# Performance work log

Hardware: AMD Instinct MI355X
Metric: run time of the kernel (lower is better)

Reference implementation:

```python
import jax, jax.numpy as jnp
import numpy as np

D, H, L, P = 256, 8, 3, 4
DH = D // H
SHAPES = np.array([[72, 96], [36, 48], [18, 24]], dtype=np.int64)
STARTS = np.array([0, 72 * 96, 72 * 96 + 36 * 48], dtype=np.int64)
NV = int((SHAPES[:, 0] * SHAPES[:, 1]).sum())  # 9072


def layer_norm(x, s, b):
    m = x.mean(-1, keepdims=True)
    v = ((x - m) ** 2).mean(-1, keepdims=True)
    return (x - m) / jnp.sqrt(v + 1e-5) * s + b


def bilinear(v, loc, Hl, Wl):
    # v: [B,H,Hl*Wl,dh]; loc: [B,Lq,H,P,2] normalized in [0,1]
    B, nH, _, dh = v.shape
    Lq, nP = loc.shape[1], loc.shape[3]
    x = loc[..., 0] * Wl - 0.5  # grid_sample align_corners=False
    y = loc[..., 1] * Hl - 0.5
    x0 = jnp.floor(x); y0 = jnp.floor(y)
    wx = x - x0; wy = y - y0

    def gather(xi, yi, w):
        valid = (xi >= 0) & (xi < Wl) & (yi >= 0) & (yi < Hl)  # padding_mode='zeros'
        xi_c = jnp.clip(xi, 0, Wl - 1).astype(jnp.int32)
        yi_c = jnp.clip(yi, 0, Hl - 1).astype(jnp.int32)
        idx = jnp.transpose(yi_c * Wl + xi_c, (0, 2, 1, 3)).reshape(B, nH, Lq * nP)
        g = jnp.take_along_axis(v, idx[..., None], axis=2).reshape(B, nH, Lq, nP, dh)
        m = (jnp.transpose(valid, (0, 2, 1, 3)).astype(v.dtype) * jnp.transpose(w, (0, 2, 1, 3)))[..., None]
        return g * m

    return (gather(x0, y0, (1 - wx) * (1 - wy)) + gather(x0 + 1, y0, wx * (1 - wy))
            + gather(x0, y0 + 1, (1 - wx) * wy) + gather(x0 + 1, y0 + 1, wx * wy))


def ms_deform_attn(query, value_in, spatial_shapes, level_start_index, key_padding_mask,
                   ref, off_w, off_b, aw_w, aw_b, vproj_w, vproj_b, oproj_w, oproj_b):
    B, Lq, _ = query.shape
    off = (query @ off_w + off_b).reshape(B, Lq, H, L, P, 2)
    aw = jax.nn.softmax((query @ aw_w + aw_b).reshape(B, Lq, H, L * P), axis=-1).reshape(B, Lq, H, L, P)
    # normalizer is [W_l, H_l] per level
    normalizer = jnp.asarray(np.stack([SHAPES[:, 1], SHAPES[:, 0]], axis=-1), dtype=query.dtype)  # [L,2]
    loc = ref[:, :, None, :, None, :] + off / normalizer[None, None, None, :, None, :]  # [B,Lq,H,L,P,2]
    value = value_in @ vproj_w + vproj_b
    value = jnp.where(key_padding_mask[:, :, None], 0.0, value)
    value = value.reshape(B, -1, H, DH).transpose(0, 2, 1, 3)  # [B,H,Nv,dh]
    acc = 0.0
    for l in range(L):
        Hl, Wl = int(spatial_shapes[l][0]), int(spatial_shapes[l][1])
        st = int(level_start_index[l])
        v_l = value[:, :, st:st + Hl * Wl]
        sampled = bilinear(v_l, loc[:, :, :, l], Hl, Wl)  # [B,H,Lq,P,dh]
        acc = acc + (sampled * jnp.transpose(aw[:, :, :, l], (0, 2, 1, 3))[..., None]).sum(axis=3)
    ctx = acc.transpose(0, 2, 1, 3).reshape(B, Lq, D)
    return ctx @ oproj_w + oproj_b


def mha(q_in, kv_in, key_padding_mask, qw, qb, kw, kb, vw, vb, ow, ob):
    B, Lq, _ = q_in.shape
    Lk = kv_in.shape[1]
    q = (q_in @ qw + qb).reshape(B, Lq, H, DH)
    k = (kv_in @ kw + kb).reshape(B, Lk, H, DH)
    v = (kv_in @ vw + vb).reshape(B, Lk, H, DH)
    scores = jnp.einsum('bqhd,bkhd->bhqk', q, k) / jnp.sqrt(jnp.asarray(DH, q.dtype))
    scores = jnp.where(key_padding_mask[:, None, None, :], -1e9, scores)
    a = jax.nn.softmax(scores, axis=-1)
    ctx = jnp.einsum('bhqk,bkhd->bqhd', a, v).reshape(B, Lq, D)
    return ctx @ ow + ob


def _forward(vis_tokens, text_tokens, vis_value,
             ref_w, ref_b, off_w, off_b, aw_w, aw_b, vproj_w, vproj_b, oproj_w, oproj_b,
             lvi_out_w, lvi_out_b, lvi_n1_s, lvi_n1_b, lvi_f1_w, lvi_f1_b, lvi_f2_w, lvi_f2_b, lvi_n2_s, lvi_n2_b,
             mha_qw, mha_qb, mha_kw, mha_kb, mha_vw, mha_vb, mha_ow, mha_ob,
             vli_out_w, vli_out_b, vli_n1_s, vli_n1_b, vli_f1_w, vli_f1_b, vli_f2_w, vli_f2_b, vli_n2_s, vli_n2_b,
             spatial_shapes, level_start_index, text_padding_mask, vis_key_padding_mask):
    B, Lt, _ = text_tokens.shape
    # --- DeformLVI: text queries multi-scale visual features ---
    ref = jax.nn.sigmoid(text_tokens @ ref_w + ref_b).reshape(B, Lt, L, 2)
    ctx = ms_deform_attn(text_tokens, vis_value, spatial_shapes, level_start_index, vis_key_padding_mask,
                         ref, off_w, off_b, aw_w, aw_b, vproj_w, vproj_b, oproj_w, oproj_b)
    t = layer_norm(text_tokens + ctx @ lvi_out_w + lvi_out_b, lvi_n1_s, lvi_n1_b)
    ffn = jax.nn.relu(t @ lvi_f1_w + lvi_f1_b) @ lvi_f2_w + lvi_f2_b
    text_out = layer_norm(t + ffn, lvi_n2_s, lvi_n2_b)
    # --- VLI: visual tokens query enriched text ---
    ctx_v = mha(vis_tokens, text_out, text_padding_mask, mha_qw, mha_qb, mha_kw, mha_kb, mha_vw, mha_vb, mha_ow, mha_ob)
    v = layer_norm(vis_tokens + ctx_v @ vli_out_w + vli_out_b, vli_n1_s, vli_n1_b)
    ffn_v = jax.nn.relu(v @ vli_f1_w + vli_f1_b) @ vli_f2_w + vli_f2_b
    vis_out = layer_norm(v + ffn_v, vli_n2_s, vli_n2_b)
    return vis_out, text_out


def setup_inputs() -> dict:
    key = jax.random.key(0)
    ks = iter(jax.random.split(key, 64))
    B, Lt = 8, 32
    w = lambda i, o: jax.random.normal(next(ks), (i, o), jnp.float32) * 0.02
    z = lambda o: jnp.zeros((o,), jnp.float32)
    inp = {
        'vis_tokens': jax.random.normal(next(ks), (B, NV, D), jnp.float32),
        'text_tokens': jax.random.normal(next(ks), (B, Lt, D), jnp.float32),
        'vis_value': jax.random.normal(next(ks), (B, NV, D), jnp.float32),
        'ref_w': w(D, L * 2), 'ref_b': z(L * 2),
        'off_w': w(D, H * L * P * 2), 'off_b': z(H * L * P * 2),
        'aw_w': w(D, H * L * P), 'aw_b': z(H * L * P),
        'vproj_w': w(D, D), 'vproj_b': z(D),
        'oproj_w': w(D, D), 'oproj_b': z(D),
        'lvi_out_w': w(D, D), 'lvi_out_b': z(D),
        'lvi_n1_s': jnp.ones((D,), jnp.float32), 'lvi_n1_b': z(D),
        'lvi_f1_w': w(D, 4 * D), 'lvi_f1_b': z(4 * D),
        'lvi_f2_w': w(4 * D, D), 'lvi_f2_b': z(D),
        'lvi_n2_s': jnp.ones((D,), jnp.float32), 'lvi_n2_b': z(D),
        'mha_qw': w(D, D), 'mha_qb': z(D),
        'mha_kw': w(D, D), 'mha_kb': z(D),
        'mha_vw': w(D, D), 'mha_vb': z(D),
        'mha_ow': w(D, D), 'mha_ob': z(D),
        'vli_out_w': w(D, D), 'vli_out_b': z(D),
        'vli_n1_s': jnp.ones((D,), jnp.float32), 'vli_n1_b': z(D),
        'vli_f1_w': w(D, 4 * D), 'vli_f1_b': z(4 * D),
        'vli_f2_w': w(4 * D, D), 'vli_f2_b': z(D),
        'vli_n2_s': jnp.ones((D,), jnp.float32), 'vli_n2_b': z(D),
        'spatial_shapes': SHAPES,
        'level_start_index': STARTS,
        'text_padding_mask': jnp.zeros((B, Lt), bool),
        'vis_key_padding_mask': jnp.zeros((B, NV), bool),
    }
    return inp


def reference(vis_tokens, text_tokens, vis_value,
              ref_w, ref_b, off_w, off_b, aw_w, aw_b, vproj_w, vproj_b, oproj_w, oproj_b,
              lvi_out_w, lvi_out_b, lvi_n1_s, lvi_n1_b, lvi_f1_w, lvi_f1_b, lvi_f2_w, lvi_f2_b, lvi_n2_s, lvi_n2_b,
              mha_qw, mha_qb, mha_kw, mha_kb, mha_vw, mha_vb, mha_ow, mha_ob,
              vli_out_w, vli_out_b, vli_n1_s, vli_n1_b, vli_f1_w, vli_f1_b, vli_f2_w, vli_f2_b, vli_n2_s, vli_n2_b,
              spatial_shapes, level_start_index, text_padding_mask, vis_key_padding_mask):
    return _forward(vis_tokens, text_tokens, vis_value,
                    ref_w, ref_b, off_w, off_b, aw_w, aw_b, vproj_w, vproj_b, oproj_w, oproj_b,
                    lvi_out_w, lvi_out_b, lvi_n1_s, lvi_n1_b, lvi_f1_w, lvi_f1_b, lvi_f2_w, lvi_f2_b, lvi_n2_s, lvi_n2_b,
                    mha_qw, mha_qb, mha_kw, mha_kb, mha_vw, mha_vb, mha_ow, mha_ob,
                    vli_out_w, vli_out_b, vli_n1_s, vli_n1_b, vli_f1_w, vli_f1_b, vli_f2_w, vli_f2_b, vli_n2_s, vli_n2_b,
                    spatial_shapes, level_start_index, text_padding_mask, vis_key_padding_mask)
```

## Files before the change

### kernel.cpp

```cpp
#include <hip/hip_runtime.h>
#include <hip/hip_bf16.h>
#include <math.h>

typedef __hip_bfloat16 bf16;
typedef unsigned short ushort_t;
typedef unsigned int uint_t;
typedef short v8s __attribute__((ext_vector_type(8)));
typedef float v4f __attribute__((ext_vector_type(4)));

#define NVTOK 9072
#define BATCH 8
#define LT 32
#define DMODEL 256
#define NHEAD 8
#define DHEAD 32
#define MVIS (BATCH*NVTOK)
#define MTEXT (BATCH*LT)
#define VISSZ 18579456ull

__device__ __forceinline__ float bf2f(ushort_t u){ return __uint_as_float(((uint_t)u)<<16); }
__device__ __forceinline__ ushort_t f2bfbits(float f){
  __hip_bfloat16 h = __float2bfloat16(f);
  union { __hip_bfloat16 h; ushort_t u; } c; c.h = h; return c.u;
}
__device__ __forceinline__ float ldin(const void* p, size_t i, int mode){
  return mode ? ((const float*)p)[i] : bf2f(((const ushort_t*)p)[i]);
}
__device__ __forceinline__ void stout(void* p, size_t i, int mode, float v){
  if (mode) ((float*)p)[i] = v; else ((ushort_t*)p)[i] = f2bfbits(v);
}

__device__ __forceinline__ void gload_lds16(const void* g, void* l){
  __builtin_amdgcn_global_load_lds(
      (const __attribute__((address_space(1))) unsigned int*)g,
      (__attribute__((address_space(3))) unsigned int*)l, 16, 0, 0);
}

__global__ void k_detect(const uint_t* __restrict__ buf, int n_avail, int* __restrict__ flag){
  __shared__ int zc, bc;
  if (threadIdx.x==0){ zc=0; bc=0; }
  __syncthreads();
  int stride = n_avail/2048; if (stride < 1) stride = 1;
  int nz=0, nb=0;
  for (int i=threadIdx.x; i<2048; i+=256){
    long long idx = (long long)i*stride;
    if (idx >= n_avail) break;
    uint_t d = buf[idx];
    uint_t lo = d & 0xFFFFu;
    int e = (int)((lo >> 7) & 0xFF);
    if (lo == 0) nz++;
    else if (e >= 90 && e <= 160) nb++;
  }
  atomicAdd(&zc, nz); atomicAdd(&bc, nb);
  __syncthreads();
  if (threadIdx.x==0){
    int mode;
    if (zc > 1024) mode = 1;
    else if (bc > 1228) mode = 0;
    else mode = 1;
    *flag = mode;
  }
}

__global__ __launch_bounds__(256) void k_transpose(
    const void* W, ushort_t* __restrict__ Wt, int K, int N,
    const int* __restrict__ mf)
{
  const int mode = *mf;
  __shared__ float tile[32][33];
  const int k0 = blockIdx.x*32, n0 = blockIdx.y*32;
  const int c = threadIdx.x & 31, r8 = threadIdx.x >> 5;
  #pragma unroll
  for (int i=0;i<4;i++){
    const int kk = r8 + i*8;
    tile[kk][c] = ldin(W, (size_t)(k0+kk)*N + n0 + c, mode);
  }
  __syncthreads();
  #pragma unroll
  for (int i=0;i<4;i++){
    const int nn = r8 + i*8;
    Wt[(size_t)(n0+nn)*K + k0 + c] = f2bfbits(tile[c][nn]);
  }
}

__global__ __launch_bounds__(256) void k_text_prep(
    const void* text,
    const void* ref_w, const void* ref_b,
    const void* off_w, const void* off_b,
    const void* aw_w,  const void* aw_b,
    float* __restrict__ loc_out, float* __restrict__ aw_out,
    const int* __restrict__ mf)
{
  const int mode = *mf;
  const int r = blockIdx.x;
  const int t = threadIdx.x;
  __shared__ float x[256];
  __shared__ float refv[6];
  __shared__ float offv[192];
  __shared__ float logit[96];
  x[t] = ldin(text, (size_t)r*256 + t, mode);
  __syncthreads();
  if (t < 192) {
    float s = 0.f;
    for (int k=0;k<256;k++) s += x[k]*ldin(off_w, (size_t)k*192+t, mode);
    offv[t] = s + ldin(off_b, t, mode);
  } else if (t < 198) {
    int j = t-192;
    float s = 0.f;
    for (int k=0;k<256;k++) s += x[k]*ldin(ref_w, (size_t)k*6+j, mode);
    s += ldin(ref_b, j, mode);
    refv[j] = 1.f/(1.f+expf(-s));
  }
  if (t < 96) {
    float s = 0.f;
    for (int k=0;k<256;k++) s += x[k]*ldin(aw_w, (size_t)k*96+t, mode);
    logit[t] = s + ldin(aw_b, t, mode);
  }
  __syncthreads();
  if (t < 8) {
    float mx = -1e30f;
    for (int j=0;j<12;j++) mx = fmaxf(mx, logit[t*12+j]);
    float e[12]; float den = 0.f;
    for (int j=0;j<12;j++){ e[j] = expf(logit[t*12+j]-mx); den += e[j]; }
    float inv = 1.f/den;
    for (int j=0;j<12;j++) aw_out[(size_t)r*96 + t*12 + j] = e[j]*inv;
  }
  if (t < 192) {
    int rem = t % 24;
    int l = rem >> 3;
    int c = t & 1;
    const float normW[3] = {96.f,48.f,24.f};
    const float normH[3] = {72.f,36.f,18.f};
    float nrm = (c==0) ? normW[l] : normH[l];
    loc_out[(size_t)r*192 + t] = refv[l*2+c] + offv[t]/nrm;
  }
}

__global__ __launch_bounds__(64) void k_deform(
    const void* vis_value, const char* __restrict__ vmask,
    const void* vproj_w, const void* vproj_b,
    const float* __restrict__ loc, const float* __restrict__ aw,
    float* __restrict__ ctx_out, const int* __restrict__ mf)
{
  const int mode = *mf;
  const int blk = blockIdx.x;
  const int r = blk >> 3;
  const int h = blk & 7;
  const int b = r >> 5;
  const int t = threadIdx.x;
  const int Hs[3] = {72,36,18};
  const int Wsz[3] = {96,48,24};
  const int stl[3] = {0,6912,8640};
  float s0=0.f,s1=0.f,s2=0.f,s3=0.f, wsum=0.f;
  for (int l=0;l<3;l++){
    for (int p=0;p<4;p++){
      const int sIdx = blk*12 + l*4 + p;
      const float a  = aw[sIdx];
      const float X = loc[sIdx*2+0]*(float)Wsz[l] - 0.5f;
      const float Y = loc[sIdx*2+1]*(float)Hs[l] - 0.5f;
      const float x0f = floorf(X), y0f = floorf(Y);
      const int x0 = (int)x0f, y0 = (int)y0f;
      const float wx = X-x0f, wy = Y-y0f;
      const float cw[4] = {(1.f-wx)*(1.f-wy), wx*(1.f-wy), (1.f-wx)*wy, wx*wy};
      const int cx[4] = {x0,x0+1,x0,x0+1};
      const int cy[4] = {y0,y0,y0+1,y0+1};
      for (int c=0;c<4;c++){
        if (cx[c]>=0 && cx[c]<Wsz[l] && cy[c]>=0 && cy[c]<Hs[l]){
          const size_t pos = (size_t)b*NVTOK + stl[l] + cy[c]*Wsz[l] + cx[c];
          if (vmask[pos]) continue;
          const float w = a*cw[c];
          wsum += w;
          const size_t base = pos*256 + t*4;
          s0 += w*ldin(vis_value, base+0, mode);
          s1 += w*ldin(vis_value, base+1, mode);
          s2 += w*ldin(vis_value, base+2, mode);
          s3 += w*ldin(vis_value, base+3, mode);
        }
      }
    }
  }
  __shared__ float sh[256];
  sh[t*4+0]=s0; sh[t*4+1]=s1; sh[t*4+2]=s2; sh[t*4+3]=s3;
  __syncthreads();
  if (t < 32) {
    const int col = h*32 + t;
    float acc = wsum * ldin(vproj_b, col, mode);
    for (int k=0;k<256;k++) acc += sh[k]*ldin(vproj_w, (size_t)k*256+col, mode);
    ctx_out[(size_t)r*256 + col] = acc;
  }
}

__device__ __forceinline__ float block_sum(float v, float* red){
  float sm = v;
  #pragma unroll
  for (int o=32;o>0;o>>=1) sm += __shfl_down(sm,o);
  const int t = threadIdx.x;
  __syncthreads();
  if ((t&63)==0) red[t>>6] = sm;
  __syncthreads();
  return red[0]+red[1]+red[2]+red[3];
}

__global__ __launch_bounds__(256) void k_mgemm(
    const void* A, size_t a_off, int a_kind,
    const ushort_t* __restrict__ Wt, const void* bias, float* __restrict__ C,
    int N, int K, int relu, const int* __restrict__ mf)
{
  const int mode = *mf;
  const int split = (a_kind==1) || (mode==1);
  __shared__ ushort_t Ah[128*32];
  __shared__ ushort_t Al[128*32];
  __shared__ ushort_t Bt[128*32];
  const int tid = threadIdx.x;
  const int gm0 = blockIdx.x*128, gn0 = blockIdx.y*128;
  const int wv = tid>>6, lane = tid&63;
  const int mh = (wv&1)*64, nh = (wv>>1)*64;
  const int r16 = lane&15, q8 = (lane>>4)*8;
  const int srow = tid>>1, sseg = (tid&1)*16;
  v4f acc[4][4];
  #pragma unroll
  for (int i=0;i<4;i++)
    #pragma unroll
    for (int j=0;j<4;j++) acc[i][j] = (v4f){0.f,0.f,0.f,0.f};

  for (int k0=0; k0<K; k0+=32){
    if (k0) __syncthreads();
    {
      const ushort_t* src = Wt + (size_t)(gn0+srow)*K + k0 + sseg;
      ((uint4*)&Bt[srow*32+sseg])[0]   = ((const uint4*)src)[0];
      ((uint4*)&Bt[srow*32+sseg+8])[0] = ((const uint4*)src)[1];
    }
    if (!split){
      const ushort_t* src = (const ushort_t*)A + a_off + (size_t)(gm0+srow)*K + k0 + sseg;
      ((uint4*)&Ah[srow*32+sseg])[0]   = ((const uint4*)src)[0];
      ((uint4*)&Ah[srow*32+sseg+8])[0] = ((const uint4*)src)[1];
    } else {
      const float* src = (const float*)A + a_off + (size_t)(gm0+srow)*K + k0 + sseg;
      #pragma unroll
      for (int v=0;v<4;v++){
        float4 f = ((const float4*)src)[v];
        float xs[4] = {f.x, f.y, f.z, f.w};
        #pragma unroll
        for (int e=0;e<4;e++){
          const int idx = srow*32 + sseg + v*4 + e;
          const ushort_t h = f2bfbits(xs[e]);
          Ah[idx] = h;
          Al[idx] = f2bfbits(xs[e] - bf2f(h));
        }
      }
    }
    __syncthreads();
    v8s af[4], bfr[4], al[4];
    #pragma unroll
    for (int mt=0;mt<4;mt++){
      af[mt] = *(const v8s*)&Ah[(mh + mt*16 + r16)*32 + q8];
      if (split) al[mt] = *(const v8s*)&Al[(mh + mt*16 + r16)*32 + q8];
    }
    #pragma unroll
    for (int nt=0;nt<4;nt++)
      bfr[nt] = *(const v8s*)&Bt[(nh + nt*16 + r16)*32 + q8];
    #pragma unroll
    for (int mt=0;mt<4;mt++){
      #pragma unroll
      for (int nt=0;nt<4;nt++){
        acc[mt][nt] = __builtin_amdgcn_mfma_f32_16x16x32_bf16(af[mt], bfr[nt], acc[mt][nt], 0, 0, 0);
        if (split)
          acc[mt][nt] = __builtin_amdgcn_mfma_f32_16x16x32_bf16(al[mt], bfr[nt], acc[mt][nt], 0, 0, 0);
      }
    }
  }
  const int rq = (lane>>4)*4;
  float bv[4];
  #pragma unroll
  for (int nt=0;nt<4;nt++) bv[nt] = ldin(bias, gn0 + nh + nt*16 + r16, mode);
  #pragma unroll
  for (int mt=0;mt<4;mt++){
    #pragma unroll
    for (int r=0;r<4;r++){
      const size_t ro = (size_t)(gm0 + mh + mt*16 + rq + r)*N + gn0 + nh + r16;
      #pragma unroll
      for (int nt=0;nt<4;nt++){
        float v = acc[mt][nt][r] + bv[nt];
        if (relu) v = fmaxf(v, 0.f);
        C[ro + nt*16] = v;
      }
    }
  }
}

__global__ __launch_bounds__(256) void k_mgemm3(
    const void* A, size_t a_off, int a_kind,
    const ushort_t* __restrict__ Wt, const void* bias,
    float* __restrict__ Cf, ushort_t* __restrict__ Chi,
    int N, int K, int relu, const int* __restrict__ mf)
{
  const int mode = *mf;
  const int rawf32 = (a_kind==0) && (mode==1);
  __shared__ ushort_t Ah[128*32];
  __shared__ ushort_t Bt[128*32];
  const int tid = threadIdx.x;
  const int nbx = gridDim.x, nby = gridDim.y;
  const int total = nbx*nby;
  const int f = blockIdx.y*nbx + blockIdx.x;
  const int qq = total>>3, rr = total&7;
  const int xcd = f&7, pos = f>>3;
  const int wg = (xcd<rr ? xcd*(qq+1) : rr*(qq+1) + (xcd-rr)*qq) + pos;
  const int gm0 = (wg / nby)*128, gn0 = (wg % nby)*128;

  const int wv = tid>>6, lane = tid&63;
  const int mh = (wv&1)*64, nh = (wv>>1)*64;
  const int r16 = lane&15, q8 = (lane>>4)*8;
  const int grow = tid>>2;
  const int gcol = (tid&3)*8;
  const int srow = tid>>1, sseg = (tid&1)*16;
  const ushort_t* Abf = (const ushort_t*)A + a_off;
  v4f acc[4][4];
  #pragma unroll
  for (int i=0;i<4;i++)
    #pragma unroll
    for (int j=0;j<4;j++) acc[i][j] = (v4f){0.f,0.f,0.f,0.f};

  for (int k0=0; k0<K; k0+=32){
    if (k0) __syncthreads();
    gload_lds16(Wt + (size_t)(gn0+grow)*K    + k0 + gcol, &Bt[grow*32      + gcol]);
    gload_lds16(Wt + (size_t)(gn0+grow+64)*K + k0 + gcol, &Bt[(grow+64)*32 + gcol]);
    if (!rawf32){
      gload_lds16(Abf + (size_t)(gm0+grow)*K    + k0 + gcol, &Ah[grow*32      + gcol]);
      gload_lds16(Abf + (size_t)(gm0+grow+64)*K + k0 + gcol, &Ah[(grow+64)*32 + gcol]);
    } else {
      const float* src = (const float*)A + a_off + (size_t)(gm0+srow)*K + k0 + sseg;
      #pragma unroll
      for (int v=0;v<4;v++){
        float4 fq = ((const float4*)src)[v];
        float xs[4] = {fq.x, fq.y, fq.z, fq.w};
        #pragma unroll
        for (int e=0;e<4;e++)
          Ah[srow*32 + sseg + v*4 + e] = f2bfbits(xs[e]);
      }
    }
    __syncthreads();
    v8s af[4], bfr[4];
    #pragma unroll
    for (int mt=0;mt<4;mt++)
      af[mt] = *(const v8s*)&Ah[(mh + mt*16 + r16)*32 + q8];
    #pragma unroll
    for (int nt=0;nt<4;nt++)
      bfr[nt] = *(const v8s*)&Bt[(nh + nt*16 + r16)*32 + q8];
    #pragma unroll
    for (int mt=0;mt<4;mt++){
      #pragma unroll
      for (int nt=0;nt<4;nt++)
        acc[mt][nt] = __builtin_amdgcn_mfma_f32_16x16x32_bf16(af[mt], bfr[nt], acc[mt][nt], 0, 0, 0);
    }
  }
  const int rq = (lane>>4)*4;
  float bv[4];
  #pragma unroll
  for (int nt=0;nt<4;nt++) bv[nt] = ldin(bias, gn0 + nh + nt*16 + r16, mode);
  const int outf = (Cf != nullptr);
  #pragma unroll
  for (int mt=0;mt<4;mt++){
    #pragma unroll
    for (int r=0;r<4;r++){
      const size_t ro = (size_t)(gm0 + mh + mt*16 + rq + r)*N + gn0 + nh + r16;
      #pragma unroll
      for (int nt=0;nt<4;nt++){
        float v = acc[mt][nt][r] + bv[nt];
        if (relu) v = fmaxf(v, 0.f);
        if (outf) Cf[ro + nt*16] = v;
        else      Chi[ro + nt*16] = f2bfbits(v);
      }
    }
  }
}

__global__ __launch_bounds__(256) void k_kvsplit(
    const float* __restrict__ kws, const float* __restrict__ vws,
    ushort_t* __restrict__ khi, ushort_t* __restrict__ klo,
    ushort_t* __restrict__ vthi, ushort_t* __restrict__ vtlo)
{
  const int row = blockIdx.x;
  const int b = row >> 5, key = row & 31;
  const int t = threadIdx.x;
  const float f = kws[(size_t)row*256 + t];
  const ushort_t fh = f2bfbits(f);
  khi[(size_t)row*256 + t] = fh;
  klo[(size_t)row*256 + t] = f2bfbits(f - bf2f(fh));
  const float g = vws[(size_t)row*256 + t];
  const ushort_t gh = f2bfbits(g);
  const size_t vt = ((size_t)b*256 + t)*32 + key;
  vthi[vt] = gh;
  vtlo[vt] = f2bfbits(g - bf2f(gh));
}

__global__ __launch_bounds__(256) void k_attn2(
    const ushort_t* __restrict__ qcH,
    ushort_t* __restrict__ aoh,
    const ushort_t* __restrict__ khi, const ushort_t* __restrict__ klo,
    const ushort_t* __restrict__ vthi, const ushort_t* __restrict__ vtlo,
    const char* __restrict__ tmask, int r0)
{
  __shared__ float P[4][16][36];
  const int tid = threadIdx.x;
  const int wv = tid>>6, lane = tid&63;
  const int lrow0 = blockIdx.x*64 + wv*16;
  const int b = (r0 + lrow0)/NVTOK;
  const int m16 = lane&15;
  const int kq = lane>>4;
  const int q8 = kq*8;
  const int key0 = m16, key1 = m16+16;
  const bool msk0 = tmask[b*LT + key0] != 0;
  const bool msk1 = tmask[b*LT + key1] != 0;
  const float scale = 0.17677669529663687f;

  for (int h=0; h<8; ++h){
    const size_t qoff = (size_t)(lrow0 + m16)*256 + h*32 + q8;
    const v8s qh = *(const v8s*)&qcH[qoff];
    const size_t kb0 = ((size_t)(b*32+key0)*256) + h*32 + q8;
    const size_t kb1 = ((size_t)(b*32+key1)*256) + h*32 + q8;
    const v8s kh0 = *(const v8s*)&khi[kb0];
    const v8s kl0 = *(const v8s*)&klo[kb0];
    const v8s kh1 = *(const v8s*)&khi[kb1];
    const v8s kl1 = *(const v8s*)&klo[kb1];
    v4f s0 = (v4f){0.f,0.f,0.f,0.f}, s1 = (v4f){0.f,0.f,0.f,0.f};
    s0 = __builtin_amdgcn_mfma_f32_16x16x32_bf16(qh, kh0, s0, 0,0,0);
    s0 = __builtin_amdgcn_mfma_f32_16x16x32_bf16(qh, kl0, s0, 0,0,0);
    s1 = __builtin_amdgcn_mfma_f32_16x16x32_bf16(qh, kh1, s1, 0,0,0);
    s1 = __builtin_amdgcn_mfma_f32_16x16x32_bf16(qh, kl1, s1, 0,0,0);
    float e0[4], e1[4], inv[4];
    #pragma unroll
    for (int r=0;r<4;r++){
      const float a0 = msk0 ? -1e9f : s0[r]*scale;
      const float a1 = msk1 ? -1e9f : s1[r]*scale;
      float mx = fmaxf(a0,a1);
      #pragma unroll
      for (int o=1;o<16;o<<=1) mx = fmaxf(mx, __shfl_xor(mx,o));
      const float x0 = __expf(a0-mx), x1 = __expf(a1-mx);
      float dn = x0+x1;
      #pragma unroll
      for (int o=1;o<16;o<<=1) dn += __shfl_xor(dn,o);
      e0[r]=x0; e1[r]=x1; inv[r] = 1.f/dn;
    }
    #pragma unroll
    for (int r=0;r<4;r++){
      P[wv][kq*4+r][key0] = e0[r];
      P[wv][kq*4+r][key1] = e1[r];
    }
    __syncthreads();
    float pv[8];
    *(float4*)&pv[0] = *(const float4*)&P[wv][m16][q8];
    *(float4*)&pv[4] = *(const float4*)&P[wv][m16][q8+4];
    v8s ph;
    #pragma unroll
    for (int j=0;j<8;j++) ph[j] = (short)f2bfbits(pv[j]);
    const size_t vb0 = ((size_t)(b*256 + h*32 + m16)*32) + q8;
    const size_t vb1 = ((size_t)(b*256 + h*32 + 16 + m16)*32) + q8;
    const v8s vh0 = *(const v8s*)&vthi[vb0];
    const v8s vl0 = *(const v8s*)&vtlo[vb0];
    const v8s vh1 = *(const v8s*)&vthi[vb1];
    const v8s vl1 = *(const v8s*)&vtlo[vb1];
    v4f o0 = (v4f){0.f,0.f,0.f,0.f}, o1 = (v4f){0.f,0.f,0.f,0.f};
    o0 = __builtin_amdgcn_mfma_f32_16x16x32_bf16(ph, vh0, o0, 0,0,0);
    o0 = __builtin_amdgcn_mfma_f32_16x16x32_bf16(ph, vl0, o0, 0,0,0);
    o1 = __builtin_amdgcn_mfma_f32_16x16x32_bf16(ph, vh1, o1, 0,0,0);
    o1 = __builtin_amdgcn_mfma_f32_16x16x32_bf16(ph, vl1, o1, 0,0,0);
    __syncthreads();
    #pragma unroll
    for (int r=0;r<4;r++){
      const size_t ro = (size_t)(lrow0 + kq*4 + r)*256 + h*32;
      aoh[ro + m16]      = f2bfbits(o0[r]*inv[r]);
      aoh[ro + 16 + m16] = f2bfbits(o1[r]*inv[r]);
    }
  }
}

__global__ __launch_bounds__(256) void k_add_ln(
    const float* __restrict__ X, const void* R, size_t r_off, int r_f32,
    void* OUT, size_t o_off, int o_f32,
    void* OUT2, size_t o2_off,
    const void* g, const void* be, const int* __restrict__ mf)
{
  const int mode = *mf;
  const int row = blockIdx.x; const int t = threadIdx.x;
  const size_t idx = (size_t)row*256 + t;
  __shared__ float red[4];
  const float rv = r_f32 ? ((const float*)R)[r_off+idx] : ldin(R, r_off+idx, mode);
  const float v = X[idx] + rv;
  const float m = block_sum(v, red) * (1.f/256.f);
  __syncthreads();
  const float d = v - m;
  const float var = block_sum(d*d, red) * (1.f/256.f);
  const float o = d*rsqrtf(var+1e-5f)*ldin(g,t,mode) + ldin(be,t,mode);
  if (o_f32) ((float*)OUT)[o_off+idx] = o;
  else       stout(OUT, o_off+idx, mode, o);
  if (OUT2)  stout(OUT2, o2_off+idx, mode, o);
}

__global__ __launch_bounds__(256) void k_add_ln_h(
    const float* __restrict__ X, const void* R, size_t r_off,
    ushort_t* __restrict__ OH,
    const void* g, const void* be, const int* __restrict__ mf)
{
  const int mode = *mf;
  const int row = blockIdx.x; const int t = threadIdx.x;
  const size_t idx = (size_t)row*256 + t;
  __shared__ float red[4];
  const float rv = ldin(R, r_off+idx, mode);
  const float v = X[idx] + rv;
  const float m = block_sum(v, red) * (1.f/256.f);
  __syncthreads();
  const float d = v - m;
  const float var = block_sum(d*d, red) * (1.f/256.f);
  const float o = d*rsqrtf(var+1e-5f)*ldin(g,t,mode) + ldin(be,t,mode);
  OH[idx] = f2bfbits(o);
}

__global__ __launch_bounds__(256) void k_add_ln_pres(
    const float* __restrict__ X,
    const ushort_t* __restrict__ RH,
    void* OUT, size_t o_off,
    const void* g, const void* be, const int* __restrict__ mf)
{
  const int mode = *mf;
  const int row = blockIdx.x; const int t = threadIdx.x;
  const size_t idx = (size_t)row*256 + t;
  __shared__ float red[4];
  const float rv = bf2f(RH[idx]);
  const float v = X[idx] + rv;
  const float m = block_sum(v, red) * (1.f/256.f);
  __syncthreads();
  const float d = v - m;
  const float var = block_sum(d*d, red) * (1.f/256.f);
  const float o = d*rsqrtf(var+1e-5f)*ldin(g,t,mode) + ldin(be,t,mode);
  stout(OUT, o_off+idx, mode, o);
}

extern "C" void kernel_launch(void* const* d_in, const int* in_sizes, int n_in,
                              void* d_out, int out_size, void* d_ws, size_t ws_size,
                              hipStream_t stream)
{
  (void)n_in; (void)out_size;
  const void* vis_tokens = d_in[0];
  const void* text_tokens= d_in[1];
  const void* vis_value  = d_in[2];
  const void* ref_w = d_in[3];  const void* ref_b = d_in[4];
  const void* off_w = d_in[5];  const void* off_b = d_in[6];
  const void* aw_w  = d_in[7];  const void* aw_b  = d_in[8];
  const void* vproj_w = d_in[9];  const void* vproj_b = d_in[10];
  const void* oproj_w = d_in[11]; const void* oproj_b = d_in[12];
  const void* lvi_out_w = d_in[13]; const void* lvi_out_b = d_in[14];
  const void* lvi_n1_s = d_in[15];  const void* lvi_n1_b = d_in[16];
  const void* lvi_f1_w = d_in[17];  const void* lvi_f1_b = d_in[18];
  const void* lvi_f2_w = d_in[19];  const void* lvi_f2_b = d_in[20];
  const void* lvi_n2_s = d_in[21];  const void* lvi_n2_b = d_in[22];
  const void* mha_qw = d_in[23]; const void* mha_qb = d_in[24];
  const void* mha_kw = d_in[25]; const void* mha_kb = d_in[26];
  const void* mha_vw = d_in[27]; const void* mha_vb = d_in[28];
  const void* mha_ow = d_in[29]; const void* mha_ob = d_in[30];
  const void* vli_out_w = d_in[31]; const void* vli_out_b = d_in[32];
  const void* vli_n1_s = d_in[33];  const void* vli_n1_b = d_in[34];
  const void* vli_f1_w = d_in[35];  const void* vli_f1_b = d_in[36];
  const void* vli_f2_w = d_in[37];  const void* vli_f2_b = d_in[38];
  const void* vli_n2_s = d_in[39];  const void* vli_n2_b = d_in[40];
  const char* tmask = (const char*)d_in[43];
  const char* vmask = (const char*)d_in[44];

  char* ws = (char*)d_ws;
  int*   flag    = (int*)  (ws + 0);
  float* loc_ws  = (float*)(ws + 256);
  float* aw_ws   = (float*)(ws + 196864);
  float* ctxt_ws = (float*)(ws + 295168);
  float* t_ws    = (float*)(ws + 557312);
  float* tout_ws = (float*)(ws + 819456);
  float* k_ws    = (float*)(ws + 1081600);
  float* v_ws    = (float*)(ws + 1343744);
  ushort_t* wtq  = (ushort_t*)(ws + 1605888ull);
  ushort_t* wto  = (ushort_t*)(ws + 1736960ull);
  ushort_t* wtf1 = (ushort_t*)(ws + 1868032ull);
  ushort_t* wtf2 = (ushort_t*)(ws + 2392320ull);
  ushort_t* wtk   = (ushort_t*)(ws + 2916608ull);
  ushort_t* wtv   = (ushort_t*)(ws + 3047680ull);
  ushort_t* wtop  = (ushort_t*)(ws + 3178752ull);
  ushort_t* wtlo  = (ushort_t*)(ws + 3309824ull);
  ushort_t* wtlf1 = (ushort_t*)(ws + 3440896ull);
  ushort_t* wtlf2 = (ushort_t*)(ws + 3965184ull);
  float* hbuf_t   = (float*)(ws + 4489472ull);
  float* ybuf     = (float*)(ws + 5538048ull);
  float* fbuf     = (float*)(ws + 5800192ull);
  ushort_t* khi   = (ushort_t*)(ws + 6062336ull);
  ushort_t* klo   = (ushort_t*)(ws + 6193408ull);
  ushort_t* vthi  = (ushort_t*)(ws + 6324480ull);
  ushort_t* vtlo  = (ushort_t*)(ws + 6455552ull);
  const size_t fe = 6586624ull;

  long long R_ll = 128;
  if (ws_size > fe) R_ll = (long long)((ws_size - fe) / 3584ull);
  if (R_ll > (long long)MVIS) R_ll = MVIS;
  R_ll &= ~127LL;
  if (R_ll < 128) R_ll = 128;
  const int R = (int)R_ll;
  ushort_t* qcH  = (ushort_t*)(ws + fe);
  float*    ubuf = (float*)   (ws + fe);
  ushort_t* v1H  = (ushort_t*)(ws + fe + (size_t)R*1024ull);
  ushort_t* hbH  = (ushort_t*)(ws + fe + (size_t)R*1536ull);
  ushort_t* aoH  = hbH;

  int ndw = in_sizes[1]/2; if (ndw < 1) ndw = 1;
  k_detect<<<1,256,0,stream>>>((const uint_t*)text_tokens, ndw, flag);

  k_transpose<<<dim3(8,8),  256,0,stream>>>(mha_qw,    wtq,   256, 256,  flag);
  k_transpose<<<dim3(8,8),  256,0,stream>>>(mha_ow,    wto,   256, 256,  flag);
  k_transpose<<<dim3(8,32), 256,0,stream>>>(vli_f1_w,  wtf1,  256, 1024, flag);
  k_transpose<<<dim3(32,8), 256,0,stream>>>(vli_f2_w,  wtf2,  1024, 256, flag);
  k_transpose<<<dim3(8,8),  256,0,stream>>>(mha_kw,    wtk,   256, 256,  flag);
  k_transpose<<<dim3(8,8),  256,0,stream>>>(mha_vw,    wtv,   256, 256,  flag);
  k_transpose<<<dim3(8,8),  256,0,stream>>>(oproj_w,   wtop,  256, 256,  flag);
  k_transpose<<<dim3(8,8),  256,0,stream>>>(lvi_out_w, wtlo,  256, 256,  flag);
  k_transpose<<<dim3(8,32), 256,0,stream>>>(lvi_f1_w,  wtlf1, 256, 1024, flag);
  k_transpose<<<dim3(32,8), 256,0,stream>>>(lvi_f2_w,  wtlf2, 1024, 256, flag);

  k_text_prep<<<MTEXT,256,0,stream>>>(text_tokens, ref_w, ref_b, off_w, off_b,
                                      aw_w, aw_b, loc_ws, aw_ws, flag);
  k_deform<<<MTEXT*NHEAD,64,0,stream>>>(vis_value, vmask, vproj_w, vproj_b,
                                        loc_ws, aw_ws, ctxt_ws, flag);

  {
    dim3 g22(2,2);
    k_mgemm<<<g22,256,0,stream>>>(ctxt_ws, 0, 1, wtop, oproj_b, ybuf, 256, 256, 0, flag);
    k_mgemm<<<g22,256,0,stream>>>(ybuf,    0, 1, wtlo, lvi_out_b, fbuf, 256, 256, 0, flag);
    k_add_ln<<<MTEXT,256,0,stream>>>(fbuf, text_tokens, 0, 0,
                                     t_ws, 0, 1, nullptr, 0, lvi_n1_s, lvi_n1_b, flag);
  }
  {
    dim3 g28(2,8), g22(2,2);
    k_mgemm<<<g28,256,0,stream>>>(t_ws,   0, 1, wtlf1, lvi_f1_b, hbuf_t, 1024, 256, 1, flag);
    k_mgemm<<<g22,256,0,stream>>>(hbuf_t, 0, 1, wtlf2, lvi_f2_b, fbuf,   256, 1024, 0, flag);
    k_add_ln<<<MTEXT,256,0,stream>>>(fbuf, t_ws, 0, 1,
                                     tout_ws, 0, 1, d_out, VISSZ, lvi_n2_s, lvi_n2_b, flag);
  }
  {
    dim3 g22(2,2);
    k_mgemm<<<g22,256,0,stream>>>(tout_ws, 0, 1, wtk, mha_kb, k_ws, 256, 256, 0, flag);
    k_mgemm<<<g22,256,0,stream>>>(tout_ws, 0, 1, wtv, mha_vb, v_ws, 256, 256, 0, flag);
    k_kvsplit<<<256,256,0,stream>>>(k_ws, v_ws, khi, klo, vthi, vtlo);
  }

  for (int r0 = 0; r0 < MVIS; r0 += R){
    const int nr = (MVIS - r0 < R) ? (MVIS - r0) : R;
    dim3 g2(nr/128, 2);
    k_mgemm3<<<g2,256,0,stream>>>(vis_tokens, (size_t)r0*256, 0,
                                  wtq, mha_qb, nullptr, qcH, 256, 256, 0, flag);
    k_attn2<<<nr/64,256,0,stream>>>(qcH, aoH, khi, klo, vthi, vtlo, tmask, r0);
    k_mgemm3<<<g2,256,0,stream>>>(aoH, 0, 2,
                                  wto, mha_ob, ubuf, nullptr, 256, 256, 0, flag);
    k_add_ln_h<<<nr,256,0,stream>>>(ubuf, vis_tokens, (size_t)r0*256,
                                    v1H, vli_n1_s, vli_n1_b, flag);
    dim3 g8(nr/128, 8);
    k_mgemm3<<<g8,256,0,stream>>>(v1H, 0, 2,
                                  wtf1, vli_f1_b, nullptr, hbH, 1024, 256, 1, flag);
    k_mgemm3<<<g2,256,0,stream>>>(hbH, 0, 2,
                                  wtf2, vli_f2_b, ubuf, nullptr, 256, 1024, 0, flag);
    k_add_ln_pres<<<nr,256,0,stream>>>(ubuf, v1H,
                                       d_out, (size_t)r0*256, vli_n2_s, vli_n2_b, flag);
  }
}
```

Measured before the change: 883.6 us.

## Fuse vision FFN up and down projections into one kernel keeping hidden in LDS

Replaces the two FFN GEMM launches (256->1024 with ReLU, then 1024->256) with a single kernel that computes each 128-column slice of the hidden activation, stores it as bf16 in swizzled shared memory, and immediately accumulates it into the output projection. This removes the round trip of the 1024-wide hidden buffer through global memory and shrinks per-row workspace so larger row chunks fit. In exchange each 128-row block does all the work with only nr/128 blocks of 512 threads, which lowers parallelism and re-reads the input and weight fragments from global memory for each hidden slice.

```diff
diff --git a/kernel.cpp b/kernel.cpp
--- a/kernel.cpp
+++ b/kernel.cpp
@@ -374,6 +374,99 @@
   }
 }
 
+__global__ __launch_bounds__(512) void k_ffn(
+    const ushort_t* __restrict__ X,
+    const ushort_t* __restrict__ W1t,
+    const void* b1,
+    const ushort_t* __restrict__ W2t,
+    const void* b2,
+    float* __restrict__ Y,
+    const int* __restrict__ mf)
+{
+  const int mode = *mf;
+  __shared__ ushort_t h[128*128];
+  const int tid = threadIdx.x;
+  const int wv = tid>>6, lane = tid&63;
+  const int r16 = lane&15, kq = lane>>4, q8 = kq*8;
+  const int rh = (wv&1)*64;
+  const int cs = (wv>>1)*32;
+  const int cq = (wv>>1)*64;
+  const int gm0 = blockIdx.x*128;
+  v4f yacc[4][4];
+  #pragma unroll
+  for (int i=0;i<4;i++)
+    #pragma unroll
+    for (int j=0;j<4;j++) yacc[i][j] = (v4f){0.f,0.f,0.f,0.f};
+
+  for (int j=0; j<8; ++j){
+    v4f hacc[4][2];
+    #pragma unroll
+    for (int i=0;i<4;i++){ hacc[i][0]=(v4f){0.f,0.f,0.f,0.f}; hacc[i][1]=(v4f){0.f,0.f,0.f,0.f}; }
+    #pragma unroll
+    for (int k=0;k<8;++k){
+      v8s af[4], bf[2];
+      #pragma unroll
+      for (int mt=0;mt<4;mt++)
+        af[mt] = *(const v8s*)&X[(size_t)(gm0 + rh + mt*16 + r16)*256 + k*32 + q8];
+      #pragma unroll
+      for (int nt=0;nt<2;nt++)
+        bf[nt] = *(const v8s*)&W1t[(size_t)(j*128 + cs + nt*16 + r16)*256 + k*32 + q8];
+      #pragma unroll
+      for (int mt=0;mt<4;mt++)
+        #pragma unroll
+        for (int nt=0;nt<2;nt++)
+          hacc[mt][nt] = __builtin_amdgcn_mfma_f32_16x16x32_bf16(af[mt], bf[nt], hacc[mt][nt], 0,0,0);
+    }
+    if (j) __syncthreads();
+    #pragma unroll
+    for (int nt=0;nt<2;nt++){
+      const int col = cs + nt*16 + r16;
+      const float bb = ldin(b1, j*128 + col, mode);
+      const int c2hi = (col*2) & ~15, c2lo = (col*2) & 15;
+      #pragma unroll
+      for (int mt=0;mt<4;mt++){
+        #pragma unroll
+        for (int r=0;r<4;r++){
+          const int row = rh + mt*16 + kq*4 + r;
+          const float v = fmaxf(hacc[mt][nt][r] + bb, 0.f);
+          const int byte = row*256 + (c2hi ^ ((row&7)<<4)) + c2lo;
+          h[byte>>1] = f2bfbits(v);
+        }
+      }
+    }
+    __syncthreads();
+    #pragma unroll
+    for (int kk=0;kk<4;++kk){
+      v8s af2[4], bf2[4];
+      #pragma unroll
+      for (int mt=0;mt<4;mt++){
+        const int row = rh + mt*16 + r16;
+        const int byte = row*256 + (((kk*32 + q8)*2) ^ ((row&7)<<4));
+        af2[mt] = *(const v8s*)&h[byte>>1];
+      }
+      #pragma unroll
+      for (int nt=0;nt<4;nt++)
+        bf2[nt] = *(const v8s*)&W2t[(size_t)(cq + nt*16 + r16)*1024 + j*128 + kk*32 + q8];
+      #pragma unroll
+      for (int mt=0;mt<4;mt++)
+        #pragma unroll
+        for (int nt=0;nt<4;nt++)
+          yacc[mt][nt] = __builtin_amdgcn_mfma_f32_16x16x32_bf16(af2[mt], bf2[nt], yacc[mt][nt], 0,0,0);
+    }
+  }
+  const int rq = kq*4;
+  #pragma unroll
+  for (int nt=0;nt<4;nt++){
+    const float bb = ldin(b2, cq + nt*16 + r16, mode);
+    #pragma unroll
+    for (int mt=0;mt<4;mt++){
+      #pragma unroll
+      for (int r=0;r<4;r++)
+        Y[(size_t)(gm0 + rh + mt*16 + rq + r)*256 + cq + nt*16 + r16] = yacc[mt][nt][r] + bb;
+    }
+  }
+}
+
 __global__ __launch_bounds__(256) void k_kvsplit(
     const float* __restrict__ kws, const float* __restrict__ vws,
     ushort_t* __restrict__ khi, ushort_t* __restrict__ klo,
@@ -594,7 +687,7 @@
   const size_t fe = 6586624ull;
 
   long long R_ll = 128;
-  if (ws_size > fe) R_ll = (long long)((ws_size - fe) / 3584ull);
+  if (ws_size > fe) R_ll = (long long)((ws_size - fe) / 2048ull);
   if (R_ll > (long long)MVIS) R_ll = MVIS;
   R_ll &= ~127LL;
   if (R_ll < 128) R_ll = 128;
@@ -602,8 +695,7 @@
   ushort_t* qcH  = (ushort_t*)(ws + fe);
   float*    ubuf = (float*)   (ws + fe);
   ushort_t* v1H  = (ushort_t*)(ws + fe + (size_t)R*1024ull);
-  ushort_t* hbH  = (ushort_t*)(ws + fe + (size_t)R*1536ull);
-  ushort_t* aoH  = hbH;
+  ushort_t* aoH  = (ushort_t*)(ws + fe + (size_t)R*1536ull);
 
   int ndw = in_sizes[1]/2; if (ndw < 1) ndw = 1;
   k_detect<<<1,256,0,stream>>>((const uint_t*)text_tokens, ndw, flag);
@@ -655,11 +747,7 @@
                                   wto, mha_ob, ubuf, nullptr, 256, 256, 0, flag);
     k_add_ln_h<<<nr,256,0,stream>>>(ubuf, vis_tokens, (size_t)r0*256,
                                     v1H, vli_n1_s, vli_n1_b, flag);
-    dim3 g8(nr/128, 8);
-    k_mgemm3<<<g8,256,0,stream>>>(v1H, 0, 2,
-                                  wtf1, vli_f1_b, nullptr, hbH, 1024, 256, 1, flag);
-    k_mgemm3<<<g2,256,0,stream>>>(hbH, 0, 2,
-                                  wtf2, vli_f2_b, ubuf, nullptr, 256, 1024, 0, flag);
+    k_ffn<<<nr/128,512,0,stream>>>(v1H, wtf1, vli_f1_b, wtf2, vli_f2_b, ubuf, flag);
     k_add_ln_pres<<<nr,256,0,stream>>>(ubuf, v1H,
                                        d_out, (size_t)r0*256, vli_n2_s, vli_n2_b, flag);
   }
```

Result: slower. 1.136 ms (+28.5%).

## Fuse residual add and LayerNorm into full-row GEMM epilogue

Applied to the files above, without the earlier changes.

Adds a GEMM kernel with 512 threads that computes a full 128x256 output tile, adds bias and residual, then runs LayerNorm in the epilogue using cross-wave reductions through shared memory. It replaces the o-projection and FFN2 GEMMs and their separate add+LN kernels, which removes the fp32 intermediate buffer round trip and two launches per chunk. The smaller workspace per row allows larger chunks. The trade-off is fewer blocks, since the grid loses its N split, and more register pressure from holding the full row tile.

```diff
diff --git a/kernel.cpp b/kernel.cpp
--- a/kernel.cpp
+++ b/kernel.cpp
@@ -374,6 +374,130 @@
   }
 }
 
+__global__ __launch_bounds__(512) void k_mgemm_ln(
+    const ushort_t* __restrict__ A,
+    const ushort_t* __restrict__ Wt, const void* bias,
+    const void* RES, size_t res_off, int res_bf16,
+    void* OUT, size_t out_off, int out_bf16,
+    const void* g, const void* be,
+    int K, const int* __restrict__ mf)
+{
+  const int mode = *mf;
+  __shared__ ushort_t Ah[128*32];
+  __shared__ ushort_t Bt[256*32];
+  __shared__ float rsum[4][128];
+  __shared__ float rsq[4][128];
+  const int tid = threadIdx.x;
+  const int gm0 = blockIdx.x*128;
+  const int wv = tid>>6, lane = tid&63;
+  const int wm = wv&1, wn = wv>>1;
+  const int mh = wm*64, nh = wn*64;
+  const int r16 = lane&15, kq = lane>>4, q8 = kq*8;
+  const int grow = tid>>2, gcol = (tid&3)*8;
+  v4f acc[4][4];
+  #pragma unroll
+  for (int i=0;i<4;i++)
+    #pragma unroll
+    for (int j=0;j<4;j++) acc[i][j] = (v4f){0.f,0.f,0.f,0.f};
+
+  for (int k0=0; k0<K; k0+=32){
+    if (k0) __syncthreads();
+    gload_lds16(A  + (size_t)(gm0+grow)*K + k0 + gcol, &Ah[grow*32 + gcol]);
+    gload_lds16(Wt + (size_t)grow*K       + k0 + gcol, &Bt[grow*32 + gcol]);
+    gload_lds16(Wt + (size_t)(128+grow)*K + k0 + gcol, &Bt[(128+grow)*32 + gcol]);
+    __syncthreads();
+    v8s af[4], bfr[4];
+    #pragma unroll
+    for (int mt=0;mt<4;mt++)
+      af[mt] = *(const v8s*)&Ah[(mh + mt*16 + r16)*32 + q8];
+    #pragma unroll
+    for (int nt=0;nt<4;nt++)
+      bfr[nt] = *(const v8s*)&Bt[(nh + nt*16 + r16)*32 + q8];
+    #pragma unroll
+    for (int mt=0;mt<4;mt++){
+      #pragma unroll
+      for (int nt=0;nt<4;nt++)
+        acc[mt][nt] = __builtin_amdgcn_mfma_f32_16x16x32_bf16(af[mt], bfr[nt], acc[mt][nt], 0, 0, 0);
+    }
+  }
+  float bv[4];
+  #pragma unroll
+  for (int nt=0;nt<4;nt++) bv[nt] = ldin(bias, nh + nt*16 + r16, mode);
+  #pragma unroll
+  for (int mt=0;mt<4;mt++){
+    #pragma unroll
+    for (int r=0;r<4;r++){
+      const int row_l = mh + mt*16 + kq*4 + r;
+      const size_t rbase = (size_t)(gm0 + row_l)*256;
+      #pragma unroll
+      for (int nt=0;nt<4;nt++){
+        const int col = nh + nt*16 + r16;
+        const float rv = res_bf16 ? bf2f(((const ushort_t*)RES)[res_off + rbase + col])
+                                  : ldin(RES, res_off + rbase + col, mode);
+        acc[mt][nt][r] = acc[mt][nt][r] + bv[nt] + rv;
+      }
+    }
+  }
+  #pragma unroll
+  for (int mt=0;mt<4;mt++){
+    #pragma unroll
+    for (int r=0;r<4;r++){
+      float s = acc[mt][0][r] + acc[mt][1][r] + acc[mt][2][r] + acc[mt][3][r];
+      #pragma unroll
+      for (int o=1;o<16;o<<=1) s += __shfl_xor(s, o);
+      if (r16==0) rsum[wn][mh + mt*16 + kq*4 + r] = s;
+    }
+  }
+  __syncthreads();
+  float mean[4][4];
+  #pragma unroll
+  for (int mt=0;mt<4;mt++){
+    #pragma unroll
+    for (int r=0;r<4;r++){
+      const int row_l = mh + mt*16 + kq*4 + r;
+      mean[mt][r] = (rsum[0][row_l]+rsum[1][row_l]+rsum[2][row_l]+rsum[3][row_l]) * (1.f/256.f);
+    }
+  }
+  #pragma unroll
+  for (int mt=0;mt<4;mt++){
+    #pragma unroll
+    for (int r=0;r<4;r++){
+      const float m = mean[mt][r];
+      float s2 = 0.f;
+      #pragma unroll
+      for (int nt=0;nt<4;nt++){ const float d = acc[mt][nt][r]-m; s2 += d*d; }
+      #pragma unroll
+      for (int o=1;o<16;o<<=1) s2 += __shfl_xor(s2, o);
+      if (r16==0) rsq[wn][mh + mt*16 + kq*4 + r] = s2;
+    }
+  }
+  __syncthreads();
+  float gv[4], bev[4];
+  #pragma unroll
+  for (int nt=0;nt<4;nt++){
+    gv[nt]  = ldin(g,  nh + nt*16 + r16, mode);
+    bev[nt] = ldin(be, nh + nt*16 + r16, mode);
+  }
+  #pragma unroll
+  for (int mt=0;mt<4;mt++){
+    #pragma unroll
+    for (int r=0;r<4;r++){
+      const int row_l = mh + mt*16 + kq*4 + r;
+      const float var = (rsq[0][row_l]+rsq[1][row_l]+rsq[2][row_l]+rsq[3][row_l]) * (1.f/256.f);
+      const float inv = rsqrtf(var + 1e-5f);
+      const float m = mean[mt][r];
+      const size_t obase = (size_t)(gm0 + row_l)*256;
+      #pragma unroll
+      for (int nt=0;nt<4;nt++){
+        const int col = nh + nt*16 + r16;
+        const float o = (acc[mt][nt][r]-m)*inv*gv[nt] + bev[nt];
+        if (out_bf16) ((ushort_t*)OUT)[obase + col] = f2bfbits(o);
+        else          stout(OUT, out_off + obase + col, mode, o);
+      }
+    }
+  }
+}
+
 __global__ __launch_bounds__(256) void k_kvsplit(
     const float* __restrict__ kws, const float* __restrict__ vws,
     ushort_t* __restrict__ khi, ushort_t* __restrict__ klo,
@@ -494,45 +618,6 @@
   if (o_f32) ((float*)OUT)[o_off+idx] = o;
   else       stout(OUT, o_off+idx, mode, o);
   if (OUT2)  stout(OUT2, o2_off+idx, mode, o);
-}
-
-__global__ __launch_bounds__(256) void k_add_ln_h(
-    const float* __restrict__ X, const void* R, size_t r_off,
-    ushort_t* __restrict__ OH,
-    const void* g, const void* be, const int* __restrict__ mf)
-{
-  const int mode = *mf;
-  const int row = blockIdx.x; const int t = threadIdx.x;
-  const size_t idx = (size_t)row*256 + t;
-  __shared__ float red[4];
-  const float rv = ldin(R, r_off+idx, mode);
-  const float v = X[idx] + rv;
-  const float m = block_sum(v, red) * (1.f/256.f);
-  __syncthreads();
-  const float d = v - m;
-  const float var = block_sum(d*d, red) * (1.f/256.f);
-  const float o = d*rsqrtf(var+1e-5f)*ldin(g,t,mode) + ldin(be,t,mode);
-  OH[idx] = f2bfbits(o);
-}
-
-__global__ __launch_bounds__(256) void k_add_ln_pres(
-    const float* __restrict__ X,
-    const ushort_t* __restrict__ RH,
-    void* OUT, size_t o_off,
-    const void* g, const void* be, const int* __restrict__ mf)
-{
-  const int mode = *mf;
-  const int row = blockIdx.x; const int t = threadIdx.x;
-  const size_t idx = (size_t)row*256 + t;
-  __shared__ float red[4];
-  const float rv = bf2f(RH[idx]);
-  const float v = X[idx] + rv;
-  const float m = block_sum(v, red) * (1.f/256.f);
-  __syncthreads();
-  const float d = v - m;
-  const float var = block_sum(d*d, red) * (1.f/256.f);
-  const float o = d*rsqrtf(var+1e-5f)*ldin(g,t,mode) + ldin(be,t,mode);
-  stout(OUT, o_off+idx, mode, o);
 }
 
 extern "C" void kernel_launch(void* const* d_in, const int* in_sizes, int n_in,
@@ -594,15 +679,14 @@
   const size_t fe = 6586624ull;
 
   long long R_ll = 128;
-  if (ws_size > fe) R_ll = (long long)((ws_size - fe) / 3584ull);
+  if (ws_size > fe) R_ll = (long long)((ws_size - fe) / 3072ull);
   if (R_ll > (long long)MVIS) R_ll = MVIS;
   R_ll &= ~127LL;
   if (R_ll < 128) R_ll = 128;
   const int R = (int)R_ll;
   ushort_t* qcH  = (ushort_t*)(ws + fe);
-  float*    ubuf = (float*)   (ws + fe);
-  ushort_t* v1H  = (ushort_t*)(ws + fe + (size_t)R*1024ull);
-  ushort_t* hbH  = (ushort_t*)(ws + fe + (size_t)R*1536ull);
+  ushort_t* v1H  = (ushort_t*)(ws + fe + (size_t)R*512ull);
+  ushort_t* hbH  = (ushort_t*)(ws + fe + (size_t)R*1024ull);
   ushort_t* aoH  = hbH;
 
   int ndw = in_sizes[1]/2; if (ndw < 1) ndw = 1;
@@ -647,20 +731,19 @@
 
   for (int r0 = 0; r0 < MVIS; r0 += R){
     const int nr = (MVIS - r0 < R) ? (MVIS - r0) : R;
-    dim3 g2(nr/128, 2);
+    dim3 g2(nr/128, 2), g8(nr/128, 8);
     k_mgemm3<<<g2,256,0,stream>>>(vis_tokens, (size_t)r0*256, 0,
                                   wtq, mha_qb, nullptr, qcH, 256, 256, 0, flag);
     k_attn2<<<nr/64,256,0,stream>>>(qcH, aoH, khi, klo, vthi, vtlo, tmask, r0);
-    k_mgemm3<<<g2,256,0,stream>>>(aoH, 0, 2,
-                                  wto, mha_ob, ubuf, nullptr, 256, 256, 0, flag);
-    k_add_ln_h<<<nr,256,0,stream>>>(ubuf, vis_tokens, (size_t)r0*256,
-                                    v1H, vli_n1_s, vli_n1_b, flag);
-    dim3 g8(nr/128, 8);
+    k_mgemm_ln<<<nr/128,512,0,stream>>>(aoH, wto, mha_ob,
+                                        vis_tokens, (size_t)r0*256, 0,
+                                        v1H, 0, 1,
+                                        vli_n1_s, vli_n1_b, 256, flag);
     k_mgemm3<<<g8,256,0,stream>>>(v1H, 0, 2,
                                   wtf1, vli_f1_b, nullptr, hbH, 1024, 256, 1, flag);
-    k_mgemm3<<<g2,256,0,stream>>>(hbH, 0, 2,
-                                  wtf2, vli_f2_b, ubuf, nullptr, 256, 1024, 0, flag);
-    k_add_ln_pres<<<nr,256,0,stream>>>(ubuf, v1H,
-                                       d_out, (size_t)r0*256, vli_n2_s, vli_n2_b, flag);
-  }
-}
+    k_mgemm_ln<<<nr/128,512,0,stream>>>(hbH, wtf2, vli_f2_b,
+                                        v1H, 0, 1,
+                                        d_out, (size_t)r0*256, 0,
+                                        vli_n2_s, vli_n2_b, 1024, flag);
+  }
+}
```

After: 903.3 us. 2.2% more time.
